# Optimization experiments

Hardware: AMD Instinct MI355X
Metric: run time of the kernel (lower is better)

The kernel has to match this reference:

```python
import jax, jax.numpy as jnp
import numpy as np

KERNEL_SIZE = 31
SIGMA = 3.0

def _gaussian_kernel2d(kernel_size, sigma):
    # Matches scipy.ndimage.gaussian_filter applied to a centered delta:
    # separable 1D Gaussian, truncated at radius = int(4*sigma + 0.5),
    # embedded in a kernel_size x kernel_size grid (zeros outside truncation).
    radius = int(4.0 * sigma + 0.5)  # scipy default truncate=4.0 -> radius 12
    x = np.arange(-radius, radius + 1, dtype=np.float64)
    k1 = np.exp(-0.5 * (x / sigma) ** 2)
    k1 /= k1.sum()
    full = np.zeros(kernel_size, dtype=np.float64)
    c = kernel_size // 2
    full[c - radius:c + radius + 1] = k1
    return np.outer(full, full).astype(np.float32)


def setup_inputs() -> dict:
    key = jax.random.key(0)
    x = jax.random.normal(key, (32, 3, 512, 512), dtype=jnp.float32)
    k2d = _gaussian_kernel2d(KERNEL_SIZE, SIGMA)
    # depthwise conv weight, OIHW with groups=3 -> O=3, I=1
    weight = jnp.asarray(np.broadcast_to(k2d[None, None], (3, 1, KERNEL_SIZE, KERNEL_SIZE)).copy())
    return {"x": x, "weight": weight}


def reference(x, weight):
    pad = KERNEL_SIZE // 2  # 15, ReflectionPad2d
    xp = jnp.pad(x, ((0, 0), (0, 0), (pad, pad), (pad, pad)), mode="reflect")
    # depthwise (groups=3) 31x31 conv, VALID padding -> output same HW as x
    out = jax.lax.conv_general_dilated(
        xp, weight,
        window_strides=(1, 1),
        padding="VALID",
        feature_group_count=3,
        dimension_numbers=("NCHW", "OIHW", "NCHW"),
    )
    return out
```

## Files before the change

kernel.cpp:

```cpp
#include <hip/hip_runtime.h>
#include <math.h>


#define IW 512
#define IH 512
#define RAD 12
#define TW 64
#define TH 32
#define RROWS (TH + 2*RAD)
#define RSTRIDE 100
#define MSTRIDE 65
#define NQ 24
#define NTASKA (RROWS * NQ)

__global__ __launch_bounds__(256)
void gauss_blur_sep3_kernel(const float* __restrict__ x,
                            const float* __restrict__ wgt,
                            float* __restrict__ out)
{
    __shared__ float raw[RROWS * RSTRIDE];
    __shared__ float mid[RROWS * MSTRIDE];
    __shared__ float k1s[13];

    const int tid = threadIdx.x;
    const int z   = blockIdx.z;
    const int ch  = z % 3;

    if (tid < 13) {
        const float* wp = wgt + ch * 961;
        k1s[tid] = wp[15 * 31 + 3 + tid] / sqrtf(wp[15 * 31 + 15]);
    }

    const int r0g = blockIdx.y * TH;
    const int c0g = blockIdx.x * TW;
    const float* __restrict__ src = x + (size_t)z * (IW * IH);

#pragma unroll
    for (int i = 0; i < 6; ++i) {
        const int u = tid + i * 256;
        if (i < 5 || u < NTASKA) {
            const int r = u / NQ;
            const int q = u - r * NQ;
            int gr = r0g + r - RAD;
            gr = gr < 0 ? -gr : (gr >= IH ? 2 * IH - 2 - gr : gr);
            const int gc = c0g - 16 + 4 * q;
            float4 f;
            if (gc >= 0 && gc <= IW - 4) {
                f = *(const float4*)(src + (size_t)gr * IW + gc);
            } else {
                float tv[4];
#pragma unroll
                for (int j = 0; j < 4; ++j) {
                    int g2 = gc + j;
                    g2 = g2 < 0 ? -g2 : (g2 >= IW ? 2 * IW - 2 - g2 : g2);
                    tv[j] = src[(size_t)gr * IW + g2];
                }
                f = make_float4(tv[0], tv[1], tv[2], tv[3]);
            }
            *(float4*)(&raw[r * RSTRIDE + 4 * q]) = f;
        }
    }
    __syncthreads();

    float kk[13];
#pragma unroll
    for (int t = 0; t < 13; ++t) kk[t] = k1s[t];

#pragma unroll
    for (int i = 0; i < 2; ++i) {
        const int task = tid + i * 256;
        if (i == 0 || task < RROWS * 8) {
            const int g = task & 7, m = task >> 3;
            const float* __restrict__ base = &raw[m * RSTRIDE + 8 * g + 4];
            float v[32];
#pragma unroll
            for (int q = 0; q < 8; ++q) {
                float4 f = *(const float4*)(base + 4 * q);
                v[4*q+0] = f.x; v[4*q+1] = f.y; v[4*q+2] = f.z; v[4*q+3] = f.w;
            }
#pragma unroll
            for (int o = 0; o < 8; ++o) {
                float acc = v[o + 12] * kk[12];
#pragma unroll
                for (int t = 0; t < 12; ++t)
                    acc = fmaf(v[o + t] + v[o + 24 - t], kk[t], acc);
                mid[m * MSTRIDE + 8 * g + o] = acc;
            }
        }
    }
    __syncthreads();

    const int c  = tid & 63;
    const int rb = (tid >> 6) * 8;

    float acc[8];
#pragma unroll
    for (int o = 0; o < 8; ++o) acc[o] = 0.f;

#pragma unroll
    for (int m2 = 0; m2 < 32; ++m2) {
        const float vv = mid[(rb + m2) * MSTRIDE + c];
#pragma unroll
        for (int o = 0; o < 8; ++o) {
            const int t = m2 - o;
            if (t >= 0 && t < 25) {
                const float w = (t <= 12) ? kk[t] : kk[24 - t];
                acc[o] = fmaf(vv, w, acc[o]);
            }
        }
    }

    float* __restrict__ dst = out + (size_t)z * (IW * IH) + (size_t)(r0g + rb) * IW + c0g + c;
#pragma unroll
    for (int o = 0; o < 8; ++o) {
        dst[(size_t)o * IW] = acc[o];
    }
}

extern "C" void kernel_launch(void* const* d_in, const int* in_sizes, int n_in,
                              void* d_out, int out_size, void* d_ws, size_t ws_size,
                              hipStream_t stream)
{
    const float* x   = (const float*)d_in[0];
    const float* wgt = (const float*)d_in[1];
    float* out = (float*)d_out;

    dim3 grid(IW / TW, IH / TH, 96);
    gauss_blur_sep3_kernel<<<grid, dim3(256), 0, stream>>>(x, wgt, out);
}
```

Before: 244.0 us.

## Load horizontal-pass inputs directly from global memory, drop raw LDS staging

The horizontal pass now reads each thread's 32-element row window straight from global memory, with reflect handling at the edges, instead of first staging the padded tile in shared memory. This removes the raw shared buffer, one barrier and the staging copy. Weights are also loaded per thread from global memory rather than through shared memory. The cost is heavily overlapping global loads, about four times the read volume, which must be absorbed by caches.

```diff
diff --git a/kernel.cpp b/kernel.cpp
--- a/kernel.cpp
+++ b/kernel.cpp
@@ -8,27 +8,26 @@
 #define TW 64
 #define TH 32
 #define RROWS (TH + 2*RAD)
-#define RSTRIDE 100
 #define MSTRIDE 65
-#define NQ 24
-#define NTASKA (RROWS * NQ)
+#define NTASKB (RROWS * 8)
 
 __global__ __launch_bounds__(256)
 void gauss_blur_sep3_kernel(const float* __restrict__ x,
                             const float* __restrict__ wgt,
                             float* __restrict__ out)
 {
-    __shared__ float raw[RROWS * RSTRIDE];
     __shared__ float mid[RROWS * MSTRIDE];
-    __shared__ float k1s[13];
 
     const int tid = threadIdx.x;
     const int z   = blockIdx.z;
     const int ch  = z % 3;
 
-    if (tid < 13) {
-        const float* wp = wgt + ch * 961;
-        k1s[tid] = wp[15 * 31 + 3 + tid] / sqrtf(wp[15 * 31 + 15]);
+    float kk[13];
+    {
+        const float* __restrict__ wp = wgt + ch * 961 + 15 * 31;
+        const float inv = 1.0f / sqrtf(wp[15]);
+#pragma unroll
+        for (int t = 0; t < 13; ++t) kk[t] = wp[3 + t] * inv;
     }
 
     const int r0g = blockIdx.y * TH;
@@ -36,47 +35,29 @@
     const float* __restrict__ src = x + (size_t)z * (IW * IH);
 
 #pragma unroll
-    for (int i = 0; i < 6; ++i) {
-        const int u = tid + i * 256;
-        if (i < 5 || u < NTASKA) {
-            const int r = u / NQ;
-            const int q = u - r * NQ;
-            int gr = r0g + r - RAD;
-            gr = gr < 0 ? -gr : (gr >= IH ? 2 * IH - 2 - gr : gr);
-            const int gc = c0g - 16 + 4 * q;
-            float4 f;
-            if (gc >= 0 && gc <= IW - 4) {
-                f = *(const float4*)(src + (size_t)gr * IW + gc);
-            } else {
-                float tv[4];
-#pragma unroll
-                for (int j = 0; j < 4; ++j) {
-                    int g2 = gc + j;
-                    g2 = g2 < 0 ? -g2 : (g2 >= IW ? 2 * IW - 2 - g2 : g2);
-                    tv[j] = src[(size_t)gr * IW + g2];
-                }
-                f = make_float4(tv[0], tv[1], tv[2], tv[3]);
-            }
-            *(float4*)(&raw[r * RSTRIDE + 4 * q]) = f;
-        }
-    }
-    __syncthreads();
-
-    float kk[13];
-#pragma unroll
-    for (int t = 0; t < 13; ++t) kk[t] = k1s[t];
-
-#pragma unroll
     for (int i = 0; i < 2; ++i) {
         const int task = tid + i * 256;
-        if (i == 0 || task < RROWS * 8) {
-            const int g = task & 7, m = task >> 3;
-            const float* __restrict__ base = &raw[m * RSTRIDE + 8 * g + 4];
+        if (i == 0 || task < NTASKB) {
+            const int g = task & 7;
+            const int m = task >> 3;
+            int gr = r0g + m - RAD;
+            gr = gr < 0 ? -gr : (gr >= IH ? 2 * IH - 2 - gr : gr);
+            const float* __restrict__ rp = src + (size_t)gr * IW;
+            const int gc0 = c0g + 8 * g - RAD;
             float v[32];
+            if (gc0 >= 0 && gc0 <= IW - 32) {
 #pragma unroll
-            for (int q = 0; q < 8; ++q) {
-                float4 f = *(const float4*)(base + 4 * q);
-                v[4*q+0] = f.x; v[4*q+1] = f.y; v[4*q+2] = f.z; v[4*q+3] = f.w;
+                for (int q = 0; q < 8; ++q) {
+                    const float4 f = *(const float4*)(rp + gc0 + 4 * q);
+                    v[4*q+0] = f.x; v[4*q+1] = f.y; v[4*q+2] = f.z; v[4*q+3] = f.w;
+                }
+            } else {
+#pragma unroll
+                for (int j = 0; j < 32; ++j) {
+                    int cc = gc0 + j;
+                    cc = cc < 0 ? -cc : (cc >= IW ? 2 * IW - 2 - cc : cc);
+                    v[j] = rp[cc];
+                }
             }
 #pragma unroll
             for (int o = 0; o < 8; ++o) {
@@ -110,7 +91,8 @@
         }
     }
 
-    float* __restrict__ dst = out + (size_t)z * (IW * IH) + (size_t)(r0g + rb) * IW + c0g + c;
+    float* __restrict__ dst = out + (size_t)z * (IW * IH)
+                            + (size_t)(r0g + rb) * IW + c0g + c;
 #pragma unroll
     for (int o = 0; o < 8; ++o) {
         dst[(size_t)o * IW] = acc[o];
```

Measured after the change: 275.4 us. 12.8% more time.
